# Kernel optimization log

Measured on AMD Instinct MI355X. Metric: run time of the kernel, lower is better.

The kernel has to match this reference:

```python
import jax, jax.numpy as jnp
import numpy as np

T, NENV, A = 256, 64, 16          # rollout steps, parallel envs, humans per env
INPUT, EMB, EDGE, RNN, OUT = 12, 64, 128, 128, 256


def setup_inputs() -> dict:
    key = jax.random.key(0)
    ks = jax.random.split(key, 10)
    s = 0.05
    pos = jax.random.normal(ks[0], (T, NENV, A, INPUT), jnp.float32)
    h_temporal = jax.random.normal(ks[1], (T, NENV, A, EDGE), jnp.float32)
    h_spatial_other = jax.random.normal(ks[2], (T, NENV, A, EDGE), jnp.float32)
    h = jnp.zeros((1, NENV, A, RNN), jnp.float32)
    masks = (jax.random.uniform(ks[3], (T, NENV)) > 0.03).astype(jnp.float32)
    W_enc = jax.random.normal(ks[4], (EMB, INPUT), jnp.float32) * s
    b_enc = jnp.zeros((EMB,), jnp.float32)
    W_edge = jax.random.normal(ks[5], (EMB, 2 * EDGE), jnp.float32) * s
    b_edge = jnp.zeros((EMB,), jnp.float32)
    W_ih = jax.random.normal(ks[6], (3 * RNN, 2 * EMB), jnp.float32) * s
    b_ih = jnp.zeros((3 * RNN,), jnp.float32)
    W_hh = jax.random.normal(ks[7], (3 * RNN, RNN), jnp.float32) * s
    b_hh = jnp.zeros((3 * RNN,), jnp.float32)
    W_out = jax.random.normal(ks[8], (OUT, RNN), jnp.float32) * s
    b_out = jnp.zeros((OUT,), jnp.float32)
    return dict(pos=pos, h_temporal=h_temporal, h_spatial_other=h_spatial_other,
                h=h, masks=masks, W_enc=W_enc, b_enc=b_enc, W_edge=W_edge,
                b_edge=b_edge, W_ih=W_ih, b_ih=b_ih, W_hh=W_hh, b_hh=b_hh,
                W_out=W_out, b_out=b_out)


def _gru_scan(x, h0, masks, W_ih, b_ih, W_hh, b_hh):
    # Equivalent to the torch has_zeros segment splitting: within a segment all
    # mask rows are 1 (identity multiply); at each segment start hxs is scaled
    # by masks[start]. Multiplying h by masks[t] every step reproduces this.
    def step(h, inp):
        x_t, m_t = inp                     # x_t: [N, A, D], m_t: [N]
        h = h * m_t[:, None, None]
        gi = x_t @ W_ih.T + b_ih           # [N, A, 3R]
        gh = h @ W_hh.T + b_hh             # [N, A, 3R]
        i_r, i_z, i_n = jnp.split(gi, 3, axis=-1)
        h_r, h_z, h_n = jnp.split(gh, 3, axis=-1)
        r = jax.nn.sigmoid(i_r + h_r)
        z = jax.nn.sigmoid(i_z + h_z)
        n = jnp.tanh(i_n + r * h_n)
        h_new = (1.0 - z) * n + z * h      # torch GRU update convention
        return h_new, h_new
    h_last, ys = jax.lax.scan(step, h0, (x, masks))
    return ys, h_last


def reference(pos, h_temporal, h_spatial_other, h, masks, W_enc, b_enc,
              W_edge, b_edge, W_ih, b_ih, W_hh, b_hh, W_out, b_out):
    # encoder: linear + relu on positions
    enc = jax.nn.relu(jnp.einsum('tnad,ed->tnae', pos, W_enc) + b_enc)
    # edge attention embed: cat(temporal, spatial) -> linear + relu
    edges = jnp.concatenate([h_temporal, h_spatial_other], axis=-1)
    emb = jax.nn.relu(jnp.einsum('tnad,ed->tnae', edges, W_edge) + b_edge)
    x = jnp.concatenate([enc, emb], axis=-1)       # [T, N, A, 2*EMB]
    ys, h_last = _gru_scan(x, h[0], masks, W_ih, b_ih, W_hh, b_hh)  # [T,N,A,R]
    out = jnp.einsum('tnar,or->tnao', ys, W_out) + b_out            # [T,N,A,OUT]
    return out, h_last[None]                       # h_new: [1, N, A, R]
```

## Files before the change

### kernel.cpp

```cpp
#include <hip/hip_runtime.h>
#include <hip/hip_bf16.h>
#include <stdint.h>

#define TT 256
#define ROWSG 1024
#define OUT_ELEMS ((size_t)TT * ROWSG * 256)


typedef __attribute__((ext_vector_type(8))) short bf16x8;
typedef __attribute__((ext_vector_type(4))) float f32x4;

__device__ __forceinline__ uint32_t pk2(float a, float b) {
    union { __hip_bfloat162 h; uint32_t u; } cv;
    cv.h = __float22bfloat162_rn(float2{a, b});
    return cv.u;
}
__device__ __forceinline__ uint16_t bf1(float a) {
    union { __hip_bfloat16 h; uint16_t u; } cv;
    cv.h = __float2bfloat16(a);
    return cv.u;
}
__device__ __forceinline__ float bf2f(uint32_t b16) {
    return __uint_as_float(b16 << 16);
}
__device__ __forceinline__ bf16x8 ld8cvt(const float* p) {
    float4 f0 = *(const float4*)p;
    float4 f1 = *(const float4*)(p + 4);
    union { bf16x8 v; uint32_t u[4]; } r;
    r.u[0] = pk2(f0.x, f0.y);
    r.u[1] = pk2(f0.z, f0.w);
    r.u[2] = pk2(f1.x, f1.y);
    r.u[3] = pk2(f1.z, f1.w);
    return r.v;
}

__global__ __launch_bounds__(256, 2) void k_embed(
    const float* __restrict__ pos, const float* __restrict__ ht,
    const float* __restrict__ hs,
    const float* __restrict__ W_enc, const float* __restrict__ b_enc,
    const float* __restrict__ W_edge, const float* __restrict__ b_edge,
    char* __restrict__ obase)
{
    const int tid = threadIdx.x;
    const int w = tid >> 6, lane = tid & 63;
    const int lr = lane & 15, lq = lane >> 4;

    __shared__ __align__(16) short xbuf[4][2048];

    bf16x8 Wenc[4];
    float benc[4];
    #pragma unroll
    for (int nt = 0; nt < 4; ++nt) {
        const int o = nt * 16 + lr;
        benc[nt] = b_enc[o];
        float v[8];
        #pragma unroll
        for (int j = 0; j < 8; ++j) v[j] = 0.f;
        const float* p = W_enc + o * 12;
        if (lq == 0) {
            float4 a = *(const float4*)p;
            float4 b = *(const float4*)(p + 4);
            v[0]=a.x; v[1]=a.y; v[2]=a.z; v[3]=a.w;
            v[4]=b.x; v[5]=b.y; v[6]=b.z; v[7]=b.w;
        } else if (lq == 1) {
            float4 a = *(const float4*)(p + 8);
            v[0]=a.x; v[1]=a.y; v[2]=a.z; v[3]=a.w;
        }
        union { bf16x8 vv; uint32_t u[4]; } f;
        f.u[0] = pk2(v[0], v[1]); f.u[1] = pk2(v[2], v[3]);
        f.u[2] = pk2(v[4], v[5]); f.u[3] = pk2(v[6], v[7]);
        Wenc[nt] = f.vv;
    }
    bf16x8 Wedge[8][4];
    float bedge[4];
    #pragma unroll
    for (int nt = 0; nt < 4; ++nt) {
        const int o = nt * 16 + lr;
        bedge[nt] = b_edge[o];
        #pragma unroll
        for (int kt = 0; kt < 8; ++kt)
            Wedge[kt][nt] = ld8cvt(W_edge + (size_t)o * 256 + kt * 32 + lq * 8);
    }

    for (int chunk = 0; chunk < 8; ++chunk) {
        const size_t F0 = (size_t)blockIdx.x * 512 + chunk * 64 + w * 16;
        const size_t row = F0 + lr;

        bf16x8 Apos;
        {
            float v[8];
            #pragma unroll
            for (int j = 0; j < 8; ++j) v[j] = 0.f;
            const float* p = pos + row * 12;
            if (lq == 0) {
                float4 a = *(const float4*)p;
                float4 b = *(const float4*)(p + 4);
                v[0]=a.x; v[1]=a.y; v[2]=a.z; v[3]=a.w;
                v[4]=b.x; v[5]=b.y; v[6]=b.z; v[7]=b.w;
            } else if (lq == 1) {
                float4 a = *(const float4*)(p + 8);
                v[0]=a.x; v[1]=a.y; v[2]=a.z; v[3]=a.w;
            }
            union { bf16x8 vv; uint32_t u[4]; } f;
            f.u[0] = pk2(v[0], v[1]); f.u[1] = pk2(v[2], v[3]);
            f.u[2] = pk2(v[4], v[5]); f.u[3] = pk2(v[6], v[7]);
            Apos = f.vv;
        }
        f32x4 enc_d[4], emb_d[4];
        #pragma unroll
        for (int nt = 0; nt < 4; ++nt) {
            f32x4 c = {benc[nt], benc[nt], benc[nt], benc[nt]};
            enc_d[nt] = __builtin_amdgcn_mfma_f32_16x16x32_bf16(Apos, Wenc[nt], c, 0, 0, 0);
            f32x4 e = {bedge[nt], bedge[nt], bedge[nt], bedge[nt]};
            emb_d[nt] = e;
        }
        #pragma unroll
        for (int kt = 0; kt < 8; ++kt) {
            bf16x8 Ae = (kt < 4)
                ? ld8cvt(ht + row * 128 + kt * 32 + lq * 8)
                : ld8cvt(hs + row * 128 + (kt - 4) * 32 + lq * 8);
            #pragma unroll
            for (int nt = 0; nt < 4; ++nt)
                emb_d[nt] = __builtin_amdgcn_mfma_f32_16x16x32_bf16(Ae, Wedge[kt][nt], emb_d[nt], 0, 0, 0);
        }
        short* xb = xbuf[w];
        #pragma unroll
        for (int nt = 0; nt < 4; ++nt) {
            #pragma unroll
            for (int r = 0; r < 4; ++r) {
                const int m = lq * 4 + r;
                const int o = nt * 16 + lr;
                xb[m * 128 + o]      = (short)bf1(fmaxf(enc_d[nt][r], 0.f));
                xb[m * 128 + 64 + o] = (short)bf1(fmaxf(emb_d[nt][r], 0.f));
            }
        }
        const uint4* src = (const uint4*)xb;
        uint4* dst = (uint4*)(obase + F0 * 1024 + 12288);
        #pragma unroll
        for (int i = 0; i < 4; ++i) dst[i * 64 + lane] = src[i * 64 + lane];
    }
}

__global__ __launch_bounds__(256, 2) void k_gi(
    const float* __restrict__ W_ih, const float* __restrict__ b_ih,
    char* __restrict__ obase)
{
    const int tid = threadIdx.x;
    const int w = tid >> 6, lane = tid & 63;
    const int lr = lane & 15, lq = lane >> 4;

    __shared__ __align__(16) char xl[16384];

    bf16x8 Wf[6][4];
    float bih[6];
    #pragma unroll
    for (int g = 0; g < 3; ++g)
        #pragma unroll
        for (int n2 = 0; n2 < 2; ++n2) {
            const int jj = g * 2 + n2;
            const int o = g * 128 + w * 32 + n2 * 16 + lr;
            bih[jj] = b_ih[o];
            #pragma unroll
            for (int kt = 0; kt < 4; ++kt)
                Wf[jj][kt] = ld8cvt(W_ih + (size_t)o * 128 + kt * 32 + lq * 8);
        }

    const int stg_m = tid >> 4, stg_kb = tid & 15;
    const int stg_off = stg_m * 256 + ((stg_kb * 16) ^ (stg_m << 4));
    int axoff[4];
    #pragma unroll
    for (int kt = 0; kt < 4; ++kt)
        axoff[kt] = lr * 256 + ((kt * 64 + lq * 16) ^ (lr << 4));

    for (int chunk = 0; chunk < 8; ++chunk) {
        const size_t F0c = (size_t)blockIdx.x * 512 + chunk * 64;
        #pragma unroll
        for (int i = 0; i < 4; ++i) {
            const uint4 val = *(const uint4*)(obase + (F0c + i * 16) * 1024 + 12288 + tid * 16);
            *(uint4*)(xl + i * 4096 + stg_off) = val;
        }
        __syncthreads();
        #pragma unroll 1
        for (int tile = 0; tile < 4; ++tile) {
            bf16x8 A[4];
            #pragma unroll
            for (int kt = 0; kt < 4; ++kt)
                A[kt] = *(const bf16x8*)(xl + tile * 4096 + axoff[kt]);
            char* ss = obase + (F0c + tile * 16) * 1024;
            #pragma unroll
            for (int jj = 0; jj < 6; ++jj) {
                f32x4 acc = {bih[jj], bih[jj], bih[jj], bih[jj]};
                #pragma unroll
                for (int kt = 0; kt < 4; ++kt)
                    acc = __builtin_amdgcn_mfma_f32_16x16x32_bf16(A[kt], Wf[jj][kt], acc, 0, 0, 0);
                const int nt = (jj >> 1) * 8 + w * 2 + (jj & 1);
                uint2 u;
                u.x = pk2(acc[0], acc[1]);
                u.y = pk2(acc[2], acc[3]);
                *(uint2*)(ss + nt * 512 + lane * 8) = u;
            }
        }
        __syncthreads();
    }
}

__global__ __launch_bounds__(256, 1) void k_scan(
    const float* __restrict__ h0, const float* __restrict__ masks,
    const float* __restrict__ W_hh, const float* __restrict__ b_hh,
    char* __restrict__ obase, float* __restrict__ dout)
{
    const int tid = threadIdx.x;
    const int w = tid >> 6, lane = tid & 63;
    const int lr = lane & 15, lq = lane >> 4;
    const int blk = blockIdx.x;
    const int r0 = blk * 16;

    __shared__ __align__(16) char hbf[2 * 4096];
    __shared__ float msk[TT];

    msk[tid] = masks[tid * 64 + blk];

    bf16x8 Wf[6][4];
    float bhh[6];
    #pragma unroll
    for (int g = 0; g < 3; ++g)
        #pragma unroll
        for (int n2 = 0; n2 < 2; ++n2) {
            const int jj = g * 2 + n2;
            const int o = g * 128 + w * 32 + n2 * 16 + lr;
            bhh[jj] = b_hh[o];
            #pragma unroll
            for (int kt = 0; kt < 4; ++kt)
                Wf[jj][kt] = ld8cvt(W_hh + (size_t)o * 128 + kt * 32 + lq * 8);
        }

    int roff[4], woff[2][4], gioff[6], ysoff[2];
    #pragma unroll
    for (int kt = 0; kt < 4; ++kt)
        roff[kt] = lr * 256 + ((kt * 64 + lq * 16) ^ (lr << 4));
    #pragma unroll
    for (int n2 = 0; n2 < 2; ++n2) {
        ysoff[n2] = (w * 32 + n2 * 16 + lr) * 32 + lq * 8;
        #pragma unroll
        for (int r = 0; r < 4; ++r) {
            const int m = lq * 4 + r;
            const int k = w * 32 + n2 * 16 + lr;
            woff[n2][r] = m * 256 + ((k * 2) ^ (m << 4));
        }
    }
    #pragma unroll
    for (int jj = 0; jj < 6; ++jj) {
        const int nt = (jj >> 1) * 8 + w * 2 + (jj & 1);
        gioff[jj] = nt * 512 + lane * 8;
    }

    __syncthreads();
    const float m0 = msk[0];

    float hold[2][4];
    #pragma unroll
    for (int n2 = 0; n2 < 2; ++n2)
        #pragma unroll
        for (int r = 0; r < 4; ++r)
            hold[n2][r] = h0[(size_t)(r0 + lq * 4 + r) * 128 + w * 32 + n2 * 16 + lr] * m0;

    {
        const int m = tid >> 4, kb = tid & 15;
        const float* hp = h0 + (size_t)(r0 + m) * 128 + kb * 8;
        float4 f0 = *(const float4*)hp;
        float4 f1 = *(const float4*)(hp + 4);
        union { bf16x8 v; uint32_t u[4]; } hv;
        hv.u[0] = pk2(f0.x * m0, f0.y * m0);
        hv.u[1] = pk2(f0.z * m0, f0.w * m0);
        hv.u[2] = pk2(f1.x * m0, f1.y * m0);
        hv.u[3] = pk2(f1.z * m0, f1.w * m0);
        *(bf16x8*)(hbf + m * 256 + ((kb * 16) ^ (m << 4))) = hv.v;
    }

    uint2 gic[6];
    {
        const char* gp = obase + (size_t)r0 * 1024;
        #pragma unroll
        for (int jj = 0; jj < 6; ++jj)
            gic[jj] = *(const uint2*)(gp + gioff[jj]);
    }
    const char* gnext = obase + (1 << 20) + (size_t)r0 * 1024;
    char* ysp = obase + (size_t)r0 * 1024 + 12288;
    char* const hbase = hbf;
    __syncthreads();

#define STEP(B, T) { \
    bf16x8 A[4]; \
    _Pragma("unroll") for (int kt = 0; kt < 4; ++kt) \
        A[kt] = *(const bf16x8*)(hbase + (B) * 4096 + roff[kt]); \
    uint2 gnx[6]; float mnx; \
    if ((T) < TT - 1) { \
        _Pragma("unroll") for (int jj = 0; jj < 6; ++jj) \
            gnx[jj] = *(const uint2*)(gnext + gioff[jj]); \
        mnx = msk[(T) + 1]; \
    } else { \
        _Pragma("unroll") for (int jj = 0; jj < 6; ++jj) { gnx[jj].x = 0u; gnx[jj].y = 0u; } \
        mnx = 1.0f; \
    } \
    f32x4 acc[6]; \
    _Pragma("unroll") for (int jj = 0; jj < 6; ++jj) { \
        f32x4 c = {bhh[jj], bhh[jj], bhh[jj], bhh[jj]}; \
        _Pragma("unroll") for (int kt = 0; kt < 4; ++kt) \
            c = __builtin_amdgcn_mfma_f32_16x16x32_bf16(A[kt], Wf[jj][kt], c, 0, 0, 0); \
        acc[jj] = c; \
    } \
    _Pragma("unroll") for (int n2 = 0; n2 < 2; ++n2) { \
        float hn[4]; \
        _Pragma("unroll") for (int r = 0; r < 4; ++r) { \
            const uint32_t urz = (r < 2) ? gic[n2].x : gic[n2].y; \
            const uint32_t uzz = (r < 2) ? gic[2 + n2].x : gic[2 + n2].y; \
            const uint32_t unn = (r < 2) ? gic[4 + n2].x : gic[4 + n2].y; \
            const float gr = bf2f((r & 1) ? (urz >> 16) : (urz & 0xffffu)); \
            const float gz = bf2f((r & 1) ? (uzz >> 16) : (uzz & 0xffffu)); \
            const float gn = bf2f((r & 1) ? (unn >> 16) : (unn & 0xffffu)); \
            const float rr = 1.f / (1.f + __expf(-(gr + acc[n2][r]))); \
            const float zz = 1.f / (1.f + __expf(-(gz + acc[2 + n2][r]))); \
            const float pre = gn + rr * acc[4 + n2][r]; \
            const float ex = __expf(2.f * pre); \
            const float nn = 1.f - 2.f / (ex + 1.f); \
            hn[r] = nn + zz * (hold[n2][r] - nn); \
        } \
        uint2 u; u.x = pk2(hn[0], hn[1]); u.y = pk2(hn[2], hn[3]); \
        *(uint2*)(ysp + ysoff[n2]) = u; \
        _Pragma("unroll") for (int r = 0; r < 4; ++r) { \
            const float hx = hn[r] * mnx; \
            hold[n2][r] = hx; \
            *(uint16_t*)(hbase + ((B) ^ 1) * 4096 + woff[n2][r]) = bf1(hx); \
        } \
    } \
    _Pragma("unroll") for (int jj = 0; jj < 6; ++jj) gic[jj] = gnx[jj]; \
    gnext += (1 << 20); ysp += (1 << 20); \
    __syncthreads(); \
}

    for (int t2 = 0; t2 < TT; t2 += 2) {
        STEP(0, t2)
        STEP(1, t2 + 1)
    }
#undef STEP

    #pragma unroll
    for (int n2 = 0; n2 < 2; ++n2)
        #pragma unroll
        for (int r = 0; r < 4; ++r)
            dout[OUT_ELEMS + (size_t)(r0 + lq * 4 + r) * 128 + w * 32 + n2 * 16 + lr] = hold[n2][r];
}

__global__ __launch_bounds__(256, 2) void k_out(
    const float* __restrict__ W_out, const float* __restrict__ b_out,
    char* __restrict__ obase)
{
    const int tid = threadIdx.x;
    const int w = tid >> 6, lane = tid & 63;
    const int lr = lane & 15, lq = lane >> 4;

    __shared__ __align__(16) uint4 ysbuf[4][256];

    bf16x8 Wf[4][4];
    float bo[4];
    #pragma unroll
    for (int ntl = 0; ntl < 4; ++ntl) {
        const int o = w * 64 + ntl * 16 + lr;
        bo[ntl] = b_out[o];
        #pragma unroll
        for (int kt = 0; kt < 4; ++kt)
            Wf[ntl][kt] = ld8cvt(W_out + (size_t)o * 128 + kt * 32 + lq * 8);
    }

    for (int it = 0; it < 8; ++it) {
        const int S0 = blockIdx.x * 32 + it * 4;
        {
            const int tb = tid >> 6, li = tid & 63;
            const uint4* src = (const uint4*)(obase + (size_t)(S0 + tb) * 16384 + 12288);
            #pragma unroll
            for (int i = 0; i < 4; ++i) ysbuf[tb][li + i * 64] = src[li + i * 64];
        }
        __syncthreads();
        #pragma unroll 1
        for (int tile = 0; tile < 4; ++tile) {
            const short* yb = (const short*)ysbuf[tile];
            bf16x8 A[4];
            #pragma unroll
            for (int kt = 0; kt < 4; ++kt) {
                bf16x8 a;
                #pragma unroll
                for (int j = 0; j < 8; ++j) {
                    const int k = kt * 32 + lq * 8 + j;
                    a[j] = yb[k * 16 + lr];
                }
                A[kt] = a;
            }
            char* ssp = obase + (size_t)(S0 + tile) * 16384;
            #pragma unroll
            for (int ntl = 0; ntl < 4; ++ntl) {
                f32x4 acc = {bo[ntl], bo[ntl], bo[ntl], bo[ntl]};
                #pragma unroll
                for (int kt = 0; kt < 4; ++kt)
                    acc = __builtin_amdgcn_mfma_f32_16x16x32_bf16(A[kt], Wf[ntl][kt], acc, 0, 0, 0);
                const int o = w * 64 + ntl * 16 + lr;
                #pragma unroll
                for (int r = 0; r < 4; ++r) {
                    const int m = lq * 4 + r;
                    *(float*)(ssp + m * 1024 + o * 4) = acc[r];
                }
            }
        }
        __syncthreads();
    }
}

extern "C" void kernel_launch(void* const* d_in, const int* in_sizes, int n_in,
                              void* d_out, int out_size, void* d_ws, size_t ws_size,
                              hipStream_t stream) {
    const float* pos    = (const float*)d_in[0];
    const float* ht     = (const float*)d_in[1];
    const float* hs     = (const float*)d_in[2];
    const float* h0     = (const float*)d_in[3];
    const float* masks  = (const float*)d_in[4];
    const float* W_enc  = (const float*)d_in[5];
    const float* b_enc  = (const float*)d_in[6];
    const float* W_edge = (const float*)d_in[7];
    const float* b_edge = (const float*)d_in[8];
    const float* W_ih   = (const float*)d_in[9];
    const float* b_ih   = (const float*)d_in[10];
    const float* W_hh   = (const float*)d_in[11];
    const float* b_hh   = (const float*)d_in[12];
    const float* W_out  = (const float*)d_in[13];
    const float* b_out  = (const float*)d_in[14];
    char*  obase = (char*)d_out;
    float* out   = (float*)d_out;

    hipLaunchKernelGGL(k_embed, dim3(512), dim3(256), 0, stream,
                       pos, ht, hs, W_enc, b_enc, W_edge, b_edge, obase);
    hipLaunchKernelGGL(k_gi, dim3(512), dim3(256), 0, stream,
                       W_ih, b_ih, obase);
    hipLaunchKernelGGL(k_scan, dim3(64), dim3(256), 0, stream,
                       h0, masks, W_hh, b_hh, obase, out);
    hipLaunchKernelGGL(k_out, dim3(512), dim3(256), 0, stream,
                       W_out, b_out, obase);
}
```

Baseline: 919.5 us.

## Split GRU scan across 4x more blocks with 4 rows each via LDS gate exchange

The recurrent scan kernel goes from 64 blocks of 16 rows to 256 blocks of 4 rows each, so more compute units take part in the serial time loop. The MFMA still runs on a 16-row tile whose unused rows are zero-padded. Only the valid rows of the accumulators are scattered through shared memory so each thread runs the gate nonlinearities for 2 elements instead of 8. Reciprocals now use the hardware rcp intrinsic. The cost is an extra barrier per step, wasted MFMA work on padding rows, and lower-precision reciprocals.

```diff
diff --git a/kernel.cpp b/kernel.cpp
--- a/kernel.cpp
+++ b/kernel.cpp
@@ -22,6 +22,9 @@
 }
 __device__ __forceinline__ float bf2f(uint32_t b16) {
     return __uint_as_float(b16 << 16);
+}
+__device__ __forceinline__ float rcpf(float x) {
+    return __builtin_amdgcn_rcpf(x);
 }
 __device__ __forceinline__ bf16x8 ld8cvt(const float* p) {
     float4 f0 = *(const float4*)p;
@@ -212,13 +215,19 @@
     const int tid = threadIdx.x;
     const int w = tid >> 6, lane = tid & 63;
     const int lr = lane & 15, lq = lane >> 4;
-    const int blk = blockIdx.x;
-    const int r0 = blk * 16;
+    const int kk = lane & 31, mm2 = lane >> 5;
+    const int b = blockIdx.x;
+    const int env = b >> 2;
+    const int p = (b & 3) * 4;
+    const int k = w * 32 + kk;
 
     __shared__ __align__(16) char hbf[2 * 4096];
+    __shared__ __align__(16) char gbuf[4 * 2304];
     __shared__ float msk[TT];
 
-    msk[tid] = masks[tid * 64 + blk];
+    msk[tid] = masks[tid * 64 + env];
+    *(uint4*)(hbf + tid * 32) = uint4{0u, 0u, 0u, 0u};
+    *(uint4*)(hbf + tid * 32 + 16) = uint4{0u, 0u, 0u, 0u};
 
     bf16x8 Wf[6][4];
     float bhh[6];
@@ -234,73 +243,56 @@
                 Wf[jj][kt] = ld8cvt(W_hh + (size_t)o * 128 + kt * 32 + lq * 8);
         }
 
-    int roff[4], woff[2][4], gioff[6], ysoff[2];
+    int roff[4];
     #pragma unroll
     for (int kt = 0; kt < 4; ++kt)
         roff[kt] = lr * 256 + ((kt * 64 + lq * 16) ^ (lr << 4));
-    #pragma unroll
-    for (int n2 = 0; n2 < 2; ++n2) {
-        ysoff[n2] = (w * 32 + n2 * 16 + lr) * 32 + lq * 8;
-        #pragma unroll
-        for (int r = 0; r < 4; ++r) {
-            const int m = lq * 4 + r;
-            const int k = w * 32 + n2 * 16 + lr;
-            woff[n2][r] = m * 256 + ((k * 2) ^ (m << 4));
-        }
-    }
-    #pragma unroll
-    for (int jj = 0; jj < 6; ++jj) {
-        const int nt = (jj >> 1) * 8 + w * 2 + (jj & 1);
-        gioff[jj] = nt * 512 + lane * 8;
+    char* const gw = gbuf + w * 2304;
+    int gioff[3];
+    #pragma unroll
+    for (int g = 0; g < 3; ++g)
+        gioff[g] = (g * 8 + w * 2 + (kk >> 4)) * 512 + ((b & 3) * 16 + (kk & 15)) * 8 + mm2 * 4;
+    const int ysoff = (k * 16 + p + 2 * mm2) * 2;
+    int hwoff[2];
+    #pragma unroll
+    for (int i = 0; i < 2; ++i) {
+        const int m = 2 * mm2 + i;
+        hwoff[i] = m * 256 + ((k * 2) ^ (m << 4));
     }
 
     __syncthreads();
     const float m0 = msk[0];
 
-    float hold[2][4];
-    #pragma unroll
-    for (int n2 = 0; n2 < 2; ++n2)
-        #pragma unroll
-        for (int r = 0; r < 4; ++r)
-            hold[n2][r] = h0[(size_t)(r0 + lq * 4 + r) * 128 + w * 32 + n2 * 16 + lr] * m0;
-
+    float hold[2];
+    #pragma unroll
+    for (int i = 0; i < 2; ++i) {
+        const int row = b * 4 + 2 * mm2 + i;
+        hold[i] = h0[(size_t)row * 128 + k] * m0;
+        *(uint16_t*)(hbf + hwoff[i]) = bf1(hold[i]);
+    }
+
+    uint32_t gic[3];
     {
-        const int m = tid >> 4, kb = tid & 15;
-        const float* hp = h0 + (size_t)(r0 + m) * 128 + kb * 8;
-        float4 f0 = *(const float4*)hp;
-        float4 f1 = *(const float4*)(hp + 4);
-        union { bf16x8 v; uint32_t u[4]; } hv;
-        hv.u[0] = pk2(f0.x * m0, f0.y * m0);
-        hv.u[1] = pk2(f0.z * m0, f0.w * m0);
-        hv.u[2] = pk2(f1.x * m0, f1.y * m0);
-        hv.u[3] = pk2(f1.z * m0, f1.w * m0);
-        *(bf16x8*)(hbf + m * 256 + ((kb * 16) ^ (m << 4))) = hv.v;
-    }
-
-    uint2 gic[6];
-    {
-        const char* gp = obase + (size_t)r0 * 1024;
-        #pragma unroll
-        for (int jj = 0; jj < 6; ++jj)
-            gic[jj] = *(const uint2*)(gp + gioff[jj]);
-    }
-    const char* gnext = obase + (1 << 20) + (size_t)r0 * 1024;
-    char* ysp = obase + (size_t)r0 * 1024 + 12288;
-    char* const hbase = hbf;
+        const char* gp = obase + (size_t)env * 16384;
+        #pragma unroll
+        for (int g = 0; g < 3; ++g)
+            gic[g] = *(const uint32_t*)(gp + gioff[g]);
+    }
+    const char* gnext = obase + (1 << 20) + (size_t)env * 16384;
+    char* ysp = obase + (size_t)env * 16384 + 12288;
     __syncthreads();
 
 #define STEP(B, T) { \
     bf16x8 A[4]; \
     _Pragma("unroll") for (int kt = 0; kt < 4; ++kt) \
-        A[kt] = *(const bf16x8*)(hbase + (B) * 4096 + roff[kt]); \
-    uint2 gnx[6]; float mnx; \
+        A[kt] = *(const bf16x8*)(hbf + (B) * 4096 + roff[kt]); \
+    uint32_t gn[3]; float mnx; \
     if ((T) < TT - 1) { \
-        _Pragma("unroll") for (int jj = 0; jj < 6; ++jj) \
-            gnx[jj] = *(const uint2*)(gnext + gioff[jj]); \
+        _Pragma("unroll") for (int g = 0; g < 3; ++g) \
+            gn[g] = *(const uint32_t*)(gnext + gioff[g]); \
         mnx = msk[(T) + 1]; \
     } else { \
-        _Pragma("unroll") for (int jj = 0; jj < 6; ++jj) { gnx[jj].x = 0u; gnx[jj].y = 0u; } \
-        mnx = 1.0f; \
+        gn[0] = gn[1] = gn[2] = 0u; mnx = 1.0f; \
     } \
     f32x4 acc[6]; \
     _Pragma("unroll") for (int jj = 0; jj < 6; ++jj) { \
@@ -309,31 +301,38 @@
             c = __builtin_amdgcn_mfma_f32_16x16x32_bf16(A[kt], Wf[jj][kt], c, 0, 0, 0); \
         acc[jj] = c; \
     } \
-    _Pragma("unroll") for (int n2 = 0; n2 < 2; ++n2) { \
-        float hn[4]; \
-        _Pragma("unroll") for (int r = 0; r < 4; ++r) { \
-            const uint32_t urz = (r < 2) ? gic[n2].x : gic[n2].y; \
-            const uint32_t uzz = (r < 2) ? gic[2 + n2].x : gic[2 + n2].y; \
-            const uint32_t unn = (r < 2) ? gic[4 + n2].x : gic[4 + n2].y; \
-            const float gr = bf2f((r & 1) ? (urz >> 16) : (urz & 0xffffu)); \
-            const float gz = bf2f((r & 1) ? (uzz >> 16) : (uzz & 0xffffu)); \
-            const float gn = bf2f((r & 1) ? (unn >> 16) : (unn & 0xffffu)); \
-            const float rr = 1.f / (1.f + __expf(-(gr + acc[n2][r]))); \
-            const float zz = 1.f / (1.f + __expf(-(gz + acc[2 + n2][r]))); \
-            const float pre = gn + rr * acc[4 + n2][r]; \
-            const float ex = __expf(2.f * pre); \
-            const float nn = 1.f - 2.f / (ex + 1.f); \
-            hn[r] = nn + zz * (hold[n2][r] - nn); \
-        } \
-        uint2 u; u.x = pk2(hn[0], hn[1]); u.y = pk2(hn[2], hn[3]); \
-        *(uint2*)(ysp + ysoff[n2]) = u; \
-        _Pragma("unroll") for (int r = 0; r < 4; ++r) { \
-            const float hx = hn[r] * mnx; \
-            hold[n2][r] = hx; \
-            *(uint16_t*)(hbase + ((B) ^ 1) * 4096 + woff[n2][r]) = bf1(hx); \
-        } \
+    if (lq == 0) { \
+        _Pragma("unroll") for (int g = 0; g < 3; ++g) \
+            _Pragma("unroll") for (int n2 = 0; n2 < 2; ++n2) { \
+                const int jj = g * 2 + n2; \
+                char* ga = gw + g * 768 + (n2 * 16 + lr) * 24; \
+                *(float2*)ga = float2{acc[jj][0], acc[jj][1]}; \
+                *(float2*)(ga + 8) = float2{acc[jj][2], acc[jj][3]}; \
+            } \
     } \
-    _Pragma("unroll") for (int jj = 0; jj < 6; ++jj) gic[jj] = gnx[jj]; \
+    __syncthreads(); \
+    const float2 ghr2 = *(const float2*)(gw + 0 * 768 + kk * 24 + mm2 * 8); \
+    const float2 ghz2 = *(const float2*)(gw + 1 * 768 + kk * 24 + mm2 * 8); \
+    const float2 ghn2 = *(const float2*)(gw + 2 * 768 + kk * 24 + mm2 * 8); \
+    float hn[2]; \
+    _Pragma("unroll") for (int i = 0; i < 2; ++i) { \
+        const float gir = bf2f(i ? (gic[0] >> 16) : (gic[0] & 0xffffu)); \
+        const float giz = bf2f(i ? (gic[1] >> 16) : (gic[1] & 0xffffu)); \
+        const float gin = bf2f(i ? (gic[2] >> 16) : (gic[2] & 0xffffu)); \
+        const float ghr = i ? ghr2.y : ghr2.x; \
+        const float ghz = i ? ghz2.y : ghz2.x; \
+        const float ghn = i ? ghn2.y : ghn2.x; \
+        const float rr = rcpf(1.f + __expf(-(gir + ghr))); \
+        const float zz = rcpf(1.f + __expf(-(giz + ghz))); \
+        const float pre = gin + rr * ghn; \
+        const float nn = 1.f - 2.f * rcpf(__expf(2.f * pre) + 1.f); \
+        hn[i] = nn + zz * (hold[i] - nn); \
+    } \
+    *(uint32_t*)(ysp + ysoff) = pk2(hn[0], hn[1]); \
+    hold[0] = hn[0] * mnx; hold[1] = hn[1] * mnx; \
+    *(uint16_t*)(hbf + ((B) ^ 1) * 4096 + hwoff[0]) = bf1(hold[0]); \
+    *(uint16_t*)(hbf + ((B) ^ 1) * 4096 + hwoff[1]) = bf1(hold[1]); \
+    gic[0] = gn[0]; gic[1] = gn[1]; gic[2] = gn[2]; \
     gnext += (1 << 20); ysp += (1 << 20); \
     __syncthreads(); \
 }
@@ -345,10 +344,8 @@
 #undef STEP
 
     #pragma unroll
-    for (int n2 = 0; n2 < 2; ++n2)
-        #pragma unroll
-        for (int r = 0; r < 4; ++r)
-            dout[OUT_ELEMS + (size_t)(r0 + lq * 4 + r) * 128 + w * 32 + n2 * 16 + lr] = hold[n2][r];
+    for (int i = 0; i < 2; ++i)
+        dout[OUT_ELEMS + (size_t)(b * 4 + 2 * mm2 + i) * 128 + k] = hold[i];
 }
 
 __global__ __launch_bounds__(256, 2) void k_out(
@@ -390,8 +387,8 @@
                 bf16x8 a;
                 #pragma unroll
                 for (int j = 0; j < 8; ++j) {
-                    const int k = kt * 32 + lq * 8 + j;
-                    a[j] = yb[k * 16 + lr];
+                    const int kx = kt * 32 + lq * 8 + j;
+                    a[j] = yb[kx * 16 + lr];
                 }
                 A[kt] = a;
             }
@@ -439,7 +436,7 @@
                        pos, ht, hs, W_enc, b_enc, W_edge, b_edge, obase);
     hipLaunchKernelGGL(k_gi, dim3(512), dim3(256), 0, stream,
                        W_ih, b_ih, obase);
-    hipLaunchKernelGGL(k_scan, dim3(64), dim3(256), 0, stream,
+    hipLaunchKernelGGL(k_scan, dim3(256), dim3(256), 0, stream,
                        h0, masks, W_hh, b_hh, obase, out);
     hipLaunchKernelGGL(k_out, dim3(512), dim3(256), 0, stream,
                        W_out, b_out, obase);
```

Result: faster. 779.9 us (-15.2%).
